# Kernel tuning notes

Measured on AMD Instinct MI355X. Metric: run time of the kernel, lower is better.

The kernel has to match this reference:

```python
import jax, jax.numpy as jnp
import numpy as np

B, L = 256, 65536
HIST, WIN = 256, 64
DIM, NPAT = 256, 64
AMP = 2.0


def setup_inputs() -> dict:
    key = jax.random.key(0)
    k1, k2, k3, k4, k5, k6 = jax.random.split(key, 6)
    x = jax.random.uniform(k1, (B, L), dtype=jnp.float32)
    avg = jax.random.uniform(k2, (B, NPAT), dtype=jnp.float32)
    avg_scores = avg - avg.mean(axis=-1, keepdims=True)
    # conv kernel (out=dim, in=1, k=history), kaiming-ish scale
    conv_w = jax.random.normal(k3, (DIM, 1, HIST), dtype=jnp.float32) * (1.0 / np.sqrt(HIST))
    conv_b = jax.random.normal(k4, (DIM,), dtype=jnp.float32) * 0.01
    # xavier-uniform keys
    lim = np.sqrt(6.0 / (DIM + NPAT))
    keys = jax.random.uniform(k5, (DIM, NPAT), minval=-lim, maxval=lim, dtype=jnp.float32)
    # shapes ~ rand * amp * 2 in [0, 4]
    shapes = jax.random.uniform(k6, (NPAT, WIN), dtype=jnp.float32) * (AMP * 2.0)
    return {"x": x, "avg_scores": avg_scores, "conv_w": conv_w, "conv_b": conv_b,
            "keys": keys, "shapes": shapes}


def reference(x, avg_scores, conv_w, conv_b, keys, shapes):
    batch, seqlen = x.shape
    n_pat = keys.shape[1]
    # Conv1d(1, dim, history, stride=window) on left-padded input, then ReLU
    # (dropout is identity at inference)
    out = jax.lax.conv_general_dilated(
        x[:, None, :], conv_w,
        window_strides=(WIN,), padding=[(HIST - 1, 0)],
        dimension_numbers=("NCH", "OIH", "NCH"))  # (B, dim, T)
    out = jax.nn.relu(out + conv_b[None, :, None])
    out = jnp.transpose(out, (2, 0, 1))  # (T, B, dim)
    # relu6(out @ keys): (T, B, n_patterns)
    attn_scores = jnp.clip(jnp.einsum("tbd,dp->tbp", out, keys), 0.0, 6.0)

    inv_p = 1.0 / n_pat

    def step(avg, score):  # avg, score: (B, n_patterns)
        prob = jax.nn.softmax(score - avg, axis=-1)
        return avg + prob - inv_p, prob

    _, probs = jax.lax.scan(step, avg_scores, attn_scores)  # probs: (T, B, P)
    attn_probs = jnp.transpose(probs, (1, 0, 2))  # (B, T, P)
    signal = jnp.einsum("btp,pw->btw", attn_probs, shapes).reshape(batch, -1)[:, :seqlen]
    return jax.nn.relu(signal - x)
```

## Files before the change

kernel.cpp:

```cpp
#include <hip/hip_runtime.h>

#define BB 256
#define LL 65536
#define TS 1024
#define HIST 256
#define WINW 64
#define DIM 256
#define NPAT 64

typedef short s8v __attribute__((ext_vector_type(8)));
typedef float f4v __attribute__((ext_vector_type(4)));

#define MFMA16(a, b, c) __builtin_amdgcn_mfma_f32_16x16x32_bf16((a), (b), (c), 0, 0, 0)
#define LOG2E 1.44269504f

__device__ __forceinline__ short bf16rne(float f) {
    unsigned u = __float_as_uint(f);
    unsigned r = (u + 0x7fffu + ((u >> 16) & 1u)) >> 16;
    return (short)r;
}
__device__ __forceinline__ float bf16tof(short h) {
    return __uint_as_float(((unsigned)(unsigned short)h) << 16);
}
__device__ __forceinline__ void split2(float f, short& hi, short& lo) {
    hi = bf16rne(f);
    lo = bf16rne(f - bf16tof(hi));
}

__global__ void prep_all(const float* __restrict__ w, short* __restrict__ wFH,
                         short* __restrict__ wFL,
                         const float* __restrict__ keys, short* __restrict__ kFH,
                         short* __restrict__ kFL,
                         const float* __restrict__ sh, short* __restrict__ sFH,
                         short* __restrict__ sFL) {
    int bid = blockIdx.x;
    s8v hv, lv;
    if (bid < 32) {
        int idx = bid * 256 + threadIdx.x;
        int d = idx & 255, qk = idx >> 8;
        int h0 = qk * 8;
#pragma unroll
        for (int j = 0; j < 8; ++j) {
            short h, l; split2(w[d * HIST + h0 + j], h, l);
            hv[j] = h; lv[j] = l;
        }
        *(s8v*)(wFH + (size_t)idx * 8) = hv;
        *(s8v*)(wFL + (size_t)idx * 8) = lv;
    } else if (bid < 40) {
        int idx = (bid - 32) * 256 + threadIdx.x;
        int p = idx & 63, qk = idx >> 6;
        int d0 = qk * 8;
#pragma unroll
        for (int j = 0; j < 8; ++j) {
            short h, l; split2(keys[(d0 + j) * NPAT + p], h, l);
            hv[j] = h; lv[j] = l;
        }
        *(s8v*)(kFH + (size_t)idx * 8) = hv;
        *(s8v*)(kFL + (size_t)idx * 8) = lv;
    } else {
        int idx = (bid - 40) * 256 + threadIdx.x;
        int ww = idx & 63, qk = idx >> 6;
        int p0 = qk * 8;
#pragma unroll
        for (int j = 0; j < 8; ++j) {
            short h, l; split2(sh[(p0 + j) * WINW + ww], h, l);
            hv[j] = h; lv[j] = l;
        }
        *(s8v*)(sFH + (size_t)idx * 8) = hv;
        *(s8v*)(sFL + (size_t)idx * 8) = lv;
    }
}

#define WELEM 2240
#define WUNIT 280

__device__ __forceinline__ int swz(int u) { return u ^ ((u >> 3) & 7); }

__launch_bounds__(256, 4)
__global__ void scores_mfma(const float* __restrict__ x,
                            const short* __restrict__ wFH, const short* __restrict__ wFL,
                            const short* __restrict__ kFH, const short* __restrict__ kFL,
                            const float* __restrict__ conv_b,
                            float* __restrict__ scoresT) {
    __shared__ __align__(16) short hidH[32 * 256], hidL[32 * 256];
    short* xsH = hidH;
    short* xsL = hidL;

    const int b = blockIdx.y, t0 = blockIdx.x * 32;
    const int tid = threadIdx.x;
    const int lane = tid & 63, wid = tid >> 6;
    const int m = lane & 15, q = lane >> 4;

    const float* xb = x + (size_t)b * LL;
    const int gbase = t0 * WINW - (HIST - 1);
    for (int i = tid; i < WELEM; i += 256) {
        int gi = gbase + i;
        float v = (gi >= 0) ? xb[gi] : 0.0f;
        short h, l; split2(v, h, l);
        int pos = (swz(i >> 3) << 3) | (i & 7);
        xsH[pos] = h; xsL[pos] = l;
    }
    __syncthreads();

    const int nb = wid * 64;
    f4v acc[2][4];
#pragma unroll
    for (int mt = 0; mt < 2; ++mt)
#pragma unroll
        for (int nt = 0; nt < 4; ++nt) acc[mt][nt] = (f4v)0.0f;

    for (int kt = 0; kt < 8; ++kt) {
        s8v aH[2], aL[2];
#pragma unroll
        for (int mt = 0; mt < 2; ++mt) {
            int row = mt * 16 + m;
            int su = swz(row * 8 + kt * 4 + q) << 3;
            aH[mt] = *(const s8v*)&xsH[su];
            aL[mt] = *(const s8v*)&xsL[su];
        }
        s8v bH[4], bL[4];
#pragma unroll
        for (int nt = 0; nt < 4; ++nt) {
            size_t bi = ((size_t)(kt * 4 + q) * 256 + nb + nt * 16 + m) * 8;
            bH[nt] = *(const s8v*)(wFH + bi);
            bL[nt] = *(const s8v*)(wFL + bi);
        }
#pragma unroll
        for (int mt = 0; mt < 2; ++mt)
#pragma unroll
            for (int nt = 0; nt < 4; ++nt)
                acc[mt][nt] = MFMA16(aH[mt], bH[nt], acc[mt][nt]);
#pragma unroll
        for (int mt = 0; mt < 2; ++mt)
#pragma unroll
            for (int nt = 0; nt < 4; ++nt)
                acc[mt][nt] = MFMA16(aL[mt], bH[nt], acc[mt][nt]);
#pragma unroll
        for (int mt = 0; mt < 2; ++mt)
#pragma unroll
            for (int nt = 0; nt < 4; ++nt)
                acc[mt][nt] = MFMA16(aH[mt], bL[nt], acc[mt][nt]);
    }
    __syncthreads();

#pragma unroll
    for (int mt = 0; mt < 2; ++mt)
#pragma unroll
        for (int nt = 0; nt < 4; ++nt) {
            int d = nb + nt * 16 + m;
            float bias = conv_b[d];
#pragma unroll
            for (int r = 0; r < 4; ++r) {
                int row = mt * 16 + q * 4 + r;
                float v = fmaxf(acc[mt][nt][r] + bias, 0.0f);
                short h, l; split2(v, h, l);
                int dd = d ^ ((row & 7) << 3);
                hidH[row * 256 + dd] = h;
                hidL[row * 256 + dd] = l;
            }
        }
    __syncthreads();

    const int pb = wid * 16;
    const int sw0 = (m & 7) << 3;
    f4v aHH[2], aLH[2], aHL[2];
#pragma unroll
    for (int mt = 0; mt < 2; ++mt) {
        aHH[mt] = (f4v)0.0f; aLH[mt] = (f4v)0.0f; aHL[mt] = (f4v)0.0f;
    }
    for (int kt = 0; kt < 8; ++kt) {
        s8v aH[2], aL[2];
#pragma unroll
        for (int mt = 0; mt < 2; ++mt) {
            int off = (mt * 16 + m) * 256 + ((kt * 32 + q * 8) ^ sw0);
            aH[mt] = *(const s8v*)&hidH[off];
            aL[mt] = *(const s8v*)&hidL[off];
        }
        size_t bi = ((size_t)(kt * 4 + q) * 64 + pb + m) * 8;
        s8v bH = *(const s8v*)(kFH + bi);
        s8v bL = *(const s8v*)(kFL + bi);
#pragma unroll
        for (int mt = 0; mt < 2; ++mt)
            aHH[mt] = MFMA16(aH[mt], bH, aHH[mt]);
#pragma unroll
        for (int mt = 0; mt < 2; ++mt)
            aLH[mt] = MFMA16(aL[mt], bH, aLH[mt]);
#pragma unroll
        for (int mt = 0; mt < 2; ++mt)
            aHL[mt] = MFMA16(aH[mt], bL, aHL[mt]);
    }
#pragma unroll
    for (int mt = 0; mt < 2; ++mt) {
        f4v s = aHH[mt] + aLH[mt] + aHL[mt];
        float4 st;
        st.x = fminf(fmaxf(s[0], 0.0f), 6.0f) * LOG2E;
        st.y = fminf(fmaxf(s[1], 0.0f), 6.0f) * LOG2E;
        st.z = fminf(fmaxf(s[2], 0.0f), 6.0f) * LOG2E;
        st.w = fminf(fmaxf(s[3], 0.0f), 6.0f) * LOG2E;
        *(float4*)&scoresT[((size_t)b * NPAT + pb + m) * TS + t0 + mt * 16 + q * 4] = st;
    }
}

template <int CTRL>
__device__ __forceinline__ float dppadd(float x) {
    int t = __builtin_amdgcn_update_dpp(0, __float_as_int(x), CTRL, 0xf, 0xf, true);
    return x + __int_as_float(t);
}

__launch_bounds__(64)
__global__ void scan_kernel(const float* __restrict__ scoresT,
                            const float* __restrict__ avg0,
                            float* __restrict__ probsT) {
    const int blk = blockIdx.x;
    const int bA = 2 * blk, bB = 2 * blk + 1;
    const int p = threadIdx.x;

    const float4* sA = (const float4*)(scoresT + ((size_t)bA * NPAT + p) * TS);
    const float4* sB = (const float4*)(scoresT + ((size_t)bB * NPAT + p) * TS);
    float4* qA = (float4*)(probsT + ((size_t)bA * NPAT + p) * TS);
    float4* qB = (float4*)(probsT + ((size_t)bB * NPAT + p) * TS);

    float avgA = avg0[bA * NPAT + p] * LOG2E;
    float avgB = avg0[bB * NPAT + p] * LOG2E;
    const float invc = LOG2E / NPAT;

    float4 bufA[4], bufB[4];
#pragma unroll
    for (int s = 0; s < 4; ++s) { bufA[s] = sA[s]; bufB[s] = sB[s]; }

    for (int base = 0; base < TS / 4; base += 4) {
#pragma unroll
        for (int s = 0; s < 4; ++s) {
            const int g = base + s;
            float4 vA = bufA[s], vB = bufB[s];
            float4 prA, prB;
            float* a = (float*)&vA;  float* bv = (float*)&vB;
            float* pa = (float*)&prA; float* pb = (float*)&prB;
#pragma unroll
            for (int j = 0; j < 4; ++j) {
                float eA = exp2f(a[j] - avgA);
                float eB = exp2f(bv[j] - avgB);
                float wA = eA, wB = eB;
                wA = dppadd<0x111>(wA); wB = dppadd<0x111>(wB);
                wA = dppadd<0x112>(wA); wB = dppadd<0x112>(wB);
                wA = dppadd<0x114>(wA); wB = dppadd<0x114>(wB);
                wA = dppadd<0x118>(wA); wB = dppadd<0x118>(wB);
                wA = dppadd<0x142>(wA); wB = dppadd<0x142>(wB);
                wA = dppadd<0x143>(wA); wB = dppadd<0x143>(wB);
                float tA = __int_as_float(__builtin_amdgcn_readlane(__float_as_int(wA), 63));
                float tB = __int_as_float(__builtin_amdgcn_readlane(__float_as_int(wB), 63));
                float prAv = eA * __builtin_amdgcn_rcpf(tA);
                float prBv = eB * __builtin_amdgcn_rcpf(tB);
                pa[j] = prAv; pb[j] = prBv;
                avgA = __builtin_fmaf(prAv, LOG2E, avgA - invc);
                avgB = __builtin_fmaf(prBv, LOG2E, avgB - invc);
            }
            if (g + 4 < TS / 4) {
                bufA[s] = sA[g + 4];
                bufB[s] = sB[g + 4];
            }
            qA[g] = prA;
            qB[g] = prB;
        }
    }
}

__launch_bounds__(256)
__global__ void signal_mfma(const float* __restrict__ probsT,
                            const short* __restrict__ sFH, const short* __restrict__ sFL,
                            const float* __restrict__ x,
                            float* __restrict__ out) {
    __shared__ __align__(16) short pH[64 * 72], pL[64 * 72];
    const int b = blockIdx.y, t0 = blockIdx.x * 64;
    const int tid = threadIdx.x;
    const int lane = tid & 63, wid = tid >> 6;
    const int m = lane & 15, q = lane >> 4;

    {
        const int pl = tid & 63, ck = tid >> 6;
        const float* src = probsT + ((size_t)b * NPAT + pl) * TS + t0 + ck * 16;
#pragma unroll
        for (int k = 0; k < 4; ++k) {
            float4 v = *(const float4*)(src + k * 4);
            float* vp = (float*)&v;
#pragma unroll
            for (int j = 0; j < 4; ++j) {
                short h, l; split2(vp[j], h, l);
                int t = ck * 16 + k * 4 + j;
                pH[t * 72 + pl] = h;
                pL[t * 72 + pl] = l;
            }
        }
    }
    __syncthreads();

    f4v acc[4];
#pragma unroll
    for (int nt = 0; nt < 4; ++nt) acc[nt] = (f4v)0.0f;

#pragma unroll
    for (int kt = 0; kt < 2; ++kt) {
        int off = (wid * 16 + m) * 72 + kt * 32 + q * 8;
        s8v aH = *(const s8v*)&pH[off];
        s8v aL = *(const s8v*)&pL[off];
#pragma unroll
        for (int nt = 0; nt < 4; ++nt) {
            size_t bi = ((size_t)(kt * 4 + q) * 64 + nt * 16 + m) * 8;
            s8v bH = *(const s8v*)(sFH + bi);
            s8v bL = *(const s8v*)(sFL + bi);
            acc[nt] = MFMA16(aH, bH, acc[nt]);
            acc[nt] = MFMA16(aL, bH, acc[nt]);
            acc[nt] = MFMA16(aH, bL, acc[nt]);
        }
    }
#pragma unroll
    for (int nt = 0; nt < 4; ++nt)
#pragma unroll
        for (int r = 0; r < 4; ++r) {
            int row = wid * 16 + q * 4 + r;
            int w = nt * 16 + m;
            size_t gi = (size_t)b * LL + (size_t)(t0 + row) * WINW + w;
            out[gi] = fmaxf(acc[nt][r] - x[gi], 0.0f);
        }
}

extern "C" void kernel_launch(void* const* d_in, const int* in_sizes, int n_in,
                              void* d_out, int out_size, void* d_ws, size_t ws_size,
                              hipStream_t stream) {
    const float* x      = (const float*)d_in[0];
    const float* avg0   = (const float*)d_in[1];
    const float* conv_w = (const float*)d_in[2];
    const float* conv_b = (const float*)d_in[3];
    const float* keys   = (const float*)d_in[4];
    const float* shapes = (const float*)d_in[5];
    float* out = (float*)d_out;

    char* ws = (char*)d_ws;
    size_t o = 0;
    float* scoresT = (float*)(ws + o); o += (size_t)BB * TS * NPAT * 4;
    float* probsT  = (float*)(ws + o); o += (size_t)BB * TS * NPAT * 4;
    short* wFH = (short*)(ws + o); o += 8192 * 16;
    short* wFL = (short*)(ws + o); o += 8192 * 16;
    short* kFH = (short*)(ws + o); o += 2048 * 16;
    short* kFL = (short*)(ws + o); o += 2048 * 16;
    short* sFH = (short*)(ws + o); o += 512 * 16;
    short* sFL = (short*)(ws + o); o += 512 * 16;

    prep_all<<<42, 256, 0, stream>>>(conv_w, wFH, wFL, keys, kFH, kFL, shapes, sFH, sFL);
    scores_mfma<<<dim3(TS / 32, BB), 256, 0, stream>>>(x, wFH, wFL, kFH, kFL, conv_b, scoresT);
    scan_kernel<<<dim3(BB / 2), 64, 0, stream>>>(scoresT, avg0, probsT);
    signal_mfma<<<dim3(TS / 64, BB), 256, 0, stream>>>(probsT, sFH, sFL, x, out);
}
```

Baseline: 416.8 us.

## Fuse softmax scan and signal MFMA into a producer-consumer kernel

```diff
diff --git a/kernel.cpp b/kernel.cpp
--- a/kernel.cpp
+++ b/kernel.cpp
@@ -72,11 +72,10 @@
 }
 
 #define WELEM 2240
-#define WUNIT 280
 
 __device__ __forceinline__ int swz(int u) { return u ^ ((u >> 3) & 7); }
 
-__launch_bounds__(256, 4)
+__launch_bounds__(256, 5)
 __global__ void scores_mfma(const float* __restrict__ x,
                             const short* __restrict__ wFH, const short* __restrict__ wFL,
                             const short* __restrict__ kFH, const short* __restrict__ kFL,
@@ -207,121 +206,123 @@
     return x + __int_as_float(t);
 }
 
-__launch_bounds__(64)
-__global__ void scan_kernel(const float* __restrict__ scoresT,
+#define CHUNK 64
+#define NCHUNK (TS / CHUNK)
+
+__launch_bounds__(128, 1)
+__global__ void scan_signal(const float* __restrict__ scoresT,
                             const float* __restrict__ avg0,
-                            float* __restrict__ probsT) {
-    const int blk = blockIdx.x;
-    const int bA = 2 * blk, bB = 2 * blk + 1;
-    const int p = threadIdx.x;
-
-    const float4* sA = (const float4*)(scoresT + ((size_t)bA * NPAT + p) * TS);
-    const float4* sB = (const float4*)(scoresT + ((size_t)bB * NPAT + p) * TS);
-    float4* qA = (float4*)(probsT + ((size_t)bA * NPAT + p) * TS);
-    float4* qB = (float4*)(probsT + ((size_t)bB * NPAT + p) * TS);
-
-    float avgA = avg0[bA * NPAT + p] * LOG2E;
-    float avgB = avg0[bB * NPAT + p] * LOG2E;
-    const float invc = LOG2E / NPAT;
-
-    float4 bufA[4], bufB[4];
-#pragma unroll
-    for (int s = 0; s < 4; ++s) { bufA[s] = sA[s]; bufB[s] = sB[s]; }
-
-    for (int base = 0; base < TS / 4; base += 4) {
-#pragma unroll
-        for (int s = 0; s < 4; ++s) {
-            const int g = base + s;
-            float4 vA = bufA[s], vB = bufB[s];
-            float4 prA, prB;
-            float* a = (float*)&vA;  float* bv = (float*)&vB;
-            float* pa = (float*)&prA; float* pb = (float*)&prB;
-#pragma unroll
-            for (int j = 0; j < 4; ++j) {
-                float eA = exp2f(a[j] - avgA);
-                float eB = exp2f(bv[j] - avgB);
-                float wA = eA, wB = eB;
-                wA = dppadd<0x111>(wA); wB = dppadd<0x111>(wB);
-                wA = dppadd<0x112>(wA); wB = dppadd<0x112>(wB);
-                wA = dppadd<0x114>(wA); wB = dppadd<0x114>(wB);
-                wA = dppadd<0x118>(wA); wB = dppadd<0x118>(wB);
-                wA = dppadd<0x142>(wA); wB = dppadd<0x142>(wB);
-                wA = dppadd<0x143>(wA); wB = dppadd<0x143>(wB);
-                float tA = __int_as_float(__builtin_amdgcn_readlane(__float_as_int(wA), 63));
-                float tB = __int_as_float(__builtin_amdgcn_readlane(__float_as_int(wB), 63));
-                float prAv = eA * __builtin_amdgcn_rcpf(tA);
-                float prBv = eB * __builtin_amdgcn_rcpf(tB);
-                pa[j] = prAv; pb[j] = prBv;
-                avgA = __builtin_fmaf(prAv, LOG2E, avgA - invc);
-                avgB = __builtin_fmaf(prBv, LOG2E, avgB - invc);
-            }
-            if (g + 4 < TS / 4) {
-                bufA[s] = sA[g + 4];
-                bufB[s] = sB[g + 4];
-            }
-            qA[g] = prA;
-            qB[g] = prB;
-        }
-    }
-}
-
-__launch_bounds__(256)
-__global__ void signal_mfma(const float* __restrict__ probsT,
                             const short* __restrict__ sFH, const short* __restrict__ sFL,
                             const float* __restrict__ x,
                             float* __restrict__ out) {
-    __shared__ __align__(16) short pH[64 * 72], pL[64 * 72];
-    const int b = blockIdx.y, t0 = blockIdx.x * 64;
+    __shared__ __align__(16) short pbH[2][CHUNK][64], pbL[2][CHUNK][64];
+
+    const int b = blockIdx.x;
     const int tid = threadIdx.x;
-    const int lane = tid & 63, wid = tid >> 6;
-    const int m = lane & 15, q = lane >> 4;
-
-    {
-        const int pl = tid & 63, ck = tid >> 6;
-        const float* src = probsT + ((size_t)b * NPAT + pl) * TS + t0 + ck * 16;
-#pragma unroll
-        for (int k = 0; k < 4; ++k) {
-            float4 v = *(const float4*)(src + k * 4);
-            float* vp = (float*)&v;
-#pragma unroll
-            for (int j = 0; j < 4; ++j) {
-                short h, l; split2(vp[j], h, l);
-                int t = ck * 16 + k * 4 + j;
-                pH[t * 72 + pl] = h;
-                pL[t * 72 + pl] = l;
+    const int wid = tid >> 6, lane = tid & 63;
+
+    if (wid == 0) {
+        const int p = lane;
+        const float4* sc = (const float4*)(scoresT + ((size_t)b * NPAT + p) * TS);
+        float avg = avg0[b * NPAT + p] * LOG2E;
+        const float invc = LOG2E / NPAT;
+
+        float4 buf[4];
+#pragma unroll
+        for (int s = 0; s < 4; ++s) buf[s] = sc[s];
+
+        for (int c = 0; c < NCHUNK; ++c) {
+            short* bH = &pbH[c & 1][0][0];
+            short* bL = &pbL[c & 1][0][0];
+            for (int kb = 0; kb < 16; kb += 4) {
+#pragma unroll
+                for (int s = 0; s < 4; ++s) {
+                    const int k = kb + s;
+                    const int g = c * 16 + k;
+                    float4 v = buf[s];
+                    float* a = (float*)&v;
+#pragma unroll
+                    for (int j = 0; j < 4; ++j) {
+                        float e = exp2f(a[j] - avg);
+                        float w = e;
+                        w = dppadd<0x111>(w);
+                        w = dppadd<0x112>(w);
+                        w = dppadd<0x114>(w);
+                        w = dppadd<0x118>(w);
+                        w = dppadd<0x142>(w);
+                        w = dppadd<0x143>(w);
+                        float t = __int_as_float(
+                            __builtin_amdgcn_readlane(__float_as_int(w), 63));
+                        float pr = e * __builtin_amdgcn_rcpf(t);
+                        avg = __builtin_fmaf(pr, LOG2E, avg - invc);
+                        short h, l; split2(pr, h, l);
+                        const int trow = k * 4 + j;
+                        const int col = p ^ ((trow & 7) << 3);
+                        bH[trow * 64 + col] = h;
+                        bL[trow * 64 + col] = l;
+                    }
+                    if (g + 4 < TS / 4) buf[s] = sc[g + 4];
+                }
             }
-        }
-    }
-    __syncthreads();
-
-    f4v acc[4];
-#pragma unroll
-    for (int nt = 0; nt < 4; ++nt) acc[nt] = (f4v)0.0f;
-
-#pragma unroll
-    for (int kt = 0; kt < 2; ++kt) {
-        int off = (wid * 16 + m) * 72 + kt * 32 + q * 8;
-        s8v aH = *(const s8v*)&pH[off];
-        s8v aL = *(const s8v*)&pL[off];
-#pragma unroll
-        for (int nt = 0; nt < 4; ++nt) {
-            size_t bi = ((size_t)(kt * 4 + q) * 64 + nt * 16 + m) * 8;
-            s8v bH = *(const s8v*)(sFH + bi);
-            s8v bL = *(const s8v*)(sFL + bi);
-            acc[nt] = MFMA16(aH, bH, acc[nt]);
-            acc[nt] = MFMA16(aL, bH, acc[nt]);
-            acc[nt] = MFMA16(aH, bL, acc[nt]);
-        }
-    }
-#pragma unroll
-    for (int nt = 0; nt < 4; ++nt)
-#pragma unroll
-        for (int r = 0; r < 4; ++r) {
-            int row = wid * 16 + q * 4 + r;
-            int w = nt * 16 + m;
-            size_t gi = (size_t)b * LL + (size_t)(t0 + row) * WINW + w;
-            out[gi] = fmaxf(acc[nt][r] - x[gi], 0.0f);
-        }
+            __syncthreads();
+        }
+        __syncthreads();
+    } else {
+        const int m = lane & 15, q = lane >> 4;
+        s8v sbH[2][4], sbL[2][4];
+#pragma unroll
+        for (int kt = 0; kt < 2; ++kt)
+#pragma unroll
+            for (int nt = 0; nt < 4; ++nt) {
+                size_t bi = ((size_t)(kt * 4 + q) * 64 + nt * 16 + m) * 8;
+                sbH[kt][nt] = *(const s8v*)(sFH + bi);
+                sbL[kt][nt] = *(const s8v*)(sFL + bi);
+            }
+        const float* xb = x + (size_t)b * LL;
+        float* ob = out + (size_t)b * LL;
+
+        __syncthreads();
+        for (int cc = 0; cc < NCHUNK; ++cc) {
+            const short* pH = &pbH[cc & 1][0][0];
+            const short* pL = &pbL[cc & 1][0][0];
+            const int t0 = cc * CHUNK;
+#pragma unroll
+            for (int mt = 0; mt < 4; ++mt) {
+                float xv[4][4];
+#pragma unroll
+                for (int nt = 0; nt < 4; ++nt)
+#pragma unroll
+                    for (int r = 0; r < 4; ++r)
+                        xv[nt][r] = xb[(size_t)(t0 + mt * 16 + q * 4 + r) * WINW +
+                                       nt * 16 + m];
+                f4v acc[4];
+#pragma unroll
+                for (int nt = 0; nt < 4; ++nt) acc[nt] = (f4v)0.0f;
+#pragma unroll
+                for (int kt = 0; kt < 2; ++kt) {
+                    const int rr = mt * 16 + m;
+                    const int col = (kt * 32 + q * 8) ^ ((m & 7) << 3);
+                    s8v aH = *(const s8v*)&pH[rr * 64 + col];
+                    s8v aL = *(const s8v*)&pL[rr * 64 + col];
+#pragma unroll
+                    for (int nt = 0; nt < 4; ++nt) {
+                        acc[nt] = MFMA16(aH, sbH[kt][nt], acc[nt]);
+                        acc[nt] = MFMA16(aL, sbH[kt][nt], acc[nt]);
+                        acc[nt] = MFMA16(aH, sbL[kt][nt], acc[nt]);
+                    }
+                }
+#pragma unroll
+                for (int nt = 0; nt < 4; ++nt)
+#pragma unroll
+                    for (int r = 0; r < 4; ++r) {
+                        size_t gi = (size_t)(t0 + mt * 16 + q * 4 + r) * WINW +
+                                    nt * 16 + m;
+                        ob[gi] = fmaxf(acc[nt][r] - xv[nt][r], 0.0f);
+                    }
+            }
+            __syncthreads();
+        }
+    }
 }
 
 extern "C" void kernel_launch(void* const* d_in, const int* in_sizes, int n_in,
@@ -338,7 +339,6 @@
     char* ws = (char*)d_ws;
     size_t o = 0;
     float* scoresT = (float*)(ws + o); o += (size_t)BB * TS * NPAT * 4;
-    float* probsT  = (float*)(ws + o); o += (size_t)BB * TS * NPAT * 4;
     short* wFH = (short*)(ws + o); o += 8192 * 16;
     short* wFL = (short*)(ws + o); o += 8192 * 16;
     short* kFH = (short*)(ws + o); o += 2048 * 16;
@@ -348,6 +348,5 @@
 
     prep_all<<<42, 256, 0, stream>>>(conv_w, wFH, wFL, keys, kFH, kFL, shapes, sFH, sFL);
     scores_mfma<<<dim3(TS / 32, BB), 256, 0, stream>>>(x, wFH, wFL, kFH, kFL, conv_b, scoresT);
-    scan_kernel<<<dim3(BB / 2), 64, 0, stream>>>(scoresT, avg0, probsT);
-    signal_mfma<<<dim3(TS / 64, BB), 256, 0, stream>>>(probsT, sFH, sFL, x, out);
-}
+    scan_signal<<<dim3(BB), 128, 0, stream>>>(scoresT, avg0, sFH, sFL, x, out);
+}
```

Measured after the change: 431.7 us. 1.04x slower.
